# Optimization experiments

Measured on AMD Instinct MI355X. Metric: run time of the kernel, lower is better.

Reference implementation:

```python
import jax, jax.numpy as jnp
import numpy as np

# --- static config (matches init_kwargs) ---
C = 384        # channels
H = 8          # num_heads
HD = C // H    # head_dim = 48
K = 1024       # patch_size (window)
BASE = 100.0   # rope_freq
MAX_POS = 4096
GRID_SIZE = 0.02
LN_EPS = 1e-5


def _interleave8(x, y, z):
    """Morton-interleave the low 8 bits of x,y,z -> 24-bit code (int32)."""
    key = jnp.zeros_like(x)
    for i in range(8):
        m = 1 << i
        key = key | ((x & m) << (2 * i + 2)) | ((y & m) << (2 * i + 1)) | ((z & m) << (2 * i))
    return key


def _serialize_points(xyz):
    """xyz: (B,3,N) -> (order (B,N) int32, grid (B,N,3) int32). Z-order sort."""
    pts = jnp.transpose(xyz, (0, 2, 1))                       # (B,N,3)
    grid = ((pts - pts.min(axis=1, keepdims=True)) / GRID_SIZE).astype(jnp.int32)
    grid = jnp.clip(grid, 0, 65535)
    gx, gy, gz = grid[..., 0], grid[..., 1], grid[..., 2]
    lo = _interleave8(gx & 255, gy & 255, gz & 255)           # low 24 bits of Morton code
    hi = _interleave8((gx >> 8) & 255, (gy >> 8) & 255, (gz >> 8) & 255)  # high word
    # 48-bit Morton order == lexsort with hi as primary key, lo secondary
    order = jax.vmap(lambda l, h: jnp.lexsort((l, h)))(lo, hi)
    return order.astype(jnp.int32), grid


def _rope_tables(d):
    inv_freq = 1.0 / (BASE ** (jnp.arange(0, d, 2, dtype=jnp.float32) / d))
    t = jnp.arange(MAX_POS, dtype=jnp.float32)
    freqs = t[:, None] * inv_freq[None, :]                    # (MAX_POS, d/2)
    freqs = jnp.concatenate([freqs, freqs], axis=-1)          # (MAX_POS, d)
    return jnp.cos(freqs), jnp.sin(freqs)


def _rotate_half(x):
    h = x.shape[-1] // 2
    return jnp.concatenate([-x[..., h:], x[..., :h]], axis=-1)


def _point_rope(tok, pos):
    """tok: (B,H,N,D) with D%3==0; pos: (B,N,3) int grid coords."""
    D = tok.shape[-1]
    d = D // 3
    pos = jnp.clip(pos, 0, MAX_POS - 1)
    cos, sin = _rope_tables(d)
    outs = []
    for axis, ch in enumerate(jnp.split(tok, 3, axis=-1)):
        p = pos[:, :, axis]                                   # (B,N)
        c = cos[p][:, None]                                   # (B,1,N,d)
        s = sin[p][:, None]
        outs.append(ch * c + _rotate_half(ch) * s)
    return jnp.concatenate(outs, axis=-1)


def _layernorm(x, g, b):
    mu = x.mean(axis=-1, keepdims=True)
    var = ((x - mu) ** 2).mean(axis=-1, keepdims=True)
    return (x - mu) * jax.lax.rsqrt(var + LN_EPS) * g + b


def _forward(x, xyz, ln1_g, ln1_b, qkv_w, qkv_b, proj_w, proj_b,
             ln2_g, ln2_b, ffn_w1, ffn_b1, ffn_w2, ffn_b2):
    B, C_, N = x.shape
    order, grid = _serialize_points(xyz)
    x_sorted = jnp.take_along_axis(x, order[:, None, :], axis=2)          # (B,C,N)
    grid_sorted = jnp.take_along_axis(grid, order[:, :, None], axis=1)    # (B,N,3)
    x_t = jnp.transpose(x_sorted, (0, 2, 1))                              # (B,N,C)
    shortcut = x_t
    xn = _layernorm(x_t, ln1_g, ln1_b)
    pad = (K - N % K) % K
    if pad > 0:
        xn = jnp.pad(xn, ((0, 0), (0, pad), (0, 0)))
        grid_sorted = jnp.pad(grid_sorted, ((0, 0), (0, pad), (0, 0)))
    Np = xn.shape[1]
    nw = Np // K
    qkv = (xn @ qkv_w + qkv_b).reshape(B, Np, 3, H, HD)
    q = jnp.transpose(qkv[:, :, 0], (0, 2, 1, 3))                         # (B,H,Np,HD)
    k = jnp.transpose(qkv[:, :, 1], (0, 2, 1, 3))
    v = jnp.transpose(qkv[:, :, 2], (0, 2, 1, 3))
    q = _point_rope(q, grid_sorted)
    k = _point_rope(k, grid_sorted)
    qw = q.reshape(B, H, nw, K, HD)
    kw = k.reshape(B, H, nw, K, HD)
    vw = v.reshape(B, H, nw, K, HD)
    scale = 1.0 / np.sqrt(HD).astype(np.float32)
    scores = jnp.einsum('bhwqd,bhwkd->bhwqk', qw, kw) * scale             # (B,H,nw,K,K)
    attn = jax.nn.softmax(scores, axis=-1)
    out = jnp.einsum('bhwqk,bhwkd->bhwqd', attn, vw)                      # (B,H,nw,K,HD)
    out = jnp.transpose(out, (0, 2, 3, 1, 4)).reshape(B, Np, C)
    out = out[:, :N]
    out = out @ proj_w + proj_b
    x_t = shortcut + out
    x_t = x_t + (jax.nn.gelu(_layernorm(x_t, ln2_g, ln2_b) @ ffn_w1 + ffn_b1,
                             approximate=False) @ ffn_w2 + ffn_b2)
    x_out = jnp.transpose(x_t, (0, 2, 1))                                 # (B,C,N)
    inv_order = jnp.argsort(order, axis=1)
    x_out = jnp.take_along_axis(x_out, inv_order[:, None, :], axis=2)
    return x_out


def setup_inputs() -> dict:
    key = jax.random.key(0)
    ks = jax.random.split(key, 12)
    B, N = 1, 16384
    s = 0.02
    return {
        'x': jax.random.normal(ks[0], (B, C, N), dtype=jnp.float32),
        'xyz': jax.random.uniform(ks[1], (B, 3, N), dtype=jnp.float32),
        'ln1_g': jnp.ones((C,), jnp.float32),
        'ln1_b': jnp.zeros((C,), jnp.float32),
        'qkv_w': jax.random.normal(ks[2], (C, 3 * C), jnp.float32) * s,
        'qkv_b': jnp.zeros((3 * C,), jnp.float32),
        'proj_w': jax.random.normal(ks[3], (C, C), jnp.float32) * s,
        'proj_b': jnp.zeros((C,), jnp.float32),
        'ln2_g': jnp.ones((C,), jnp.float32),
        'ln2_b': jnp.zeros((C,), jnp.float32),
        'ffn_w1': jax.random.normal(ks[4], (C, 4 * C), jnp.float32) * s,
        'ffn_b1': jnp.zeros((4 * C,), jnp.float32),
        'ffn_w2': jax.random.normal(ks[5], (4 * C, C), jnp.float32) * s,
        'ffn_b2': jnp.zeros((C,), jnp.float32),
    }


def reference(x, xyz, ln1_g, ln1_b, qkv_w, qkv_b, proj_w, proj_b,
              ln2_g, ln2_b, ffn_w1, ffn_b1, ffn_w2, ffn_b2):
    return _forward(x, xyz, ln1_g, ln1_b, qkv_w, qkv_b, proj_w, proj_b,
                    ln2_g, ln2_b, ffn_w1, ffn_b1, ffn_w2, ffn_b2)
```

## Files before the change

kernel.cpp:

```cpp
#include <hip/hip_runtime.h>
#include <hip/hip_bf16.h>

typedef unsigned short u16;
typedef unsigned int u32;
typedef unsigned long long u64;
typedef __attribute__((ext_vector_type(8))) short s16x8;
typedef __attribute__((ext_vector_type(4))) short s16x4;
typedef __attribute__((ext_vector_type(8))) unsigned short u16x8;
typedef __attribute__((ext_vector_type(4))) unsigned short u16x4;
typedef __attribute__((ext_vector_type(4))) float fx4;
typedef __attribute__((ext_vector_type(4))) unsigned int ux4;
typedef __attribute__((ext_vector_type(2))) unsigned int ux2;

__device__ __forceinline__ float bf2f(u16 u){ u32 x=((u32)u)<<16; return __builtin_bit_cast(float,x); }
__device__ __forceinline__ u16 f2bf(float f){ u32 x=__builtin_bit_cast(u32,f); return (u16)((x + 0x7FFFu + ((x>>16)&1u))>>16); }
__device__ __forceinline__ u32 cvtpk(float lo, float hi){
  u32 r; asm("v_cvt_pk_bf16_f32 %0, %1, %2" : "=v"(r) : "v"(lo), "v"(hi)); return r;
}

__device__ __forceinline__ s16x8 ld_bf8(const u16* p){
  s16x4 lo = *(const s16x4*)p;
  s16x4 hi = *(const s16x4*)(p+4);
  s16x8 r;
  r[0]=lo[0]; r[1]=lo[1]; r[2]=lo[2]; r[3]=lo[3];
  r[4]=hi[0]; r[5]=hi[1]; r[6]=hi[2]; r[7]=hi[3];
  return r;
}

__device__ __forceinline__ void gload16(const void* g, void* l){
  __builtin_amdgcn_global_load_lds((__attribute__((address_space(1))) void*)g,
                                   (__attribute__((address_space(3))) void*)l, 16, 0, 0);
}

__device__ __forceinline__ u64 spread3(u32 v){
  u64 x = v & 0xFFFFull;
  x = (x | (x<<32)) & 0x001f00000000ffffull;
  x = (x | (x<<16)) & 0x001f0000ff0000ffull;
  x = (x | (x<<8))  & 0x100f00f00f00f00full;
  x = (x | (x<<4))  & 0x10c30c30c30c30c3ull;
  x = (x | (x<<2))  & 0x1249249249249249ull;
  return x;
}

__global__ __launch_bounds__(256) void min3_kernel(const float* __restrict__ xyz, u32* __restrict__ mins, int N)
{
  int i = blockIdx.x*256 + threadIdx.x;
  float v0 = xyz[i], v1 = xyz[N+i], v2 = xyz[2*N+i];
  #pragma unroll
  for (int s=1;s<64;s<<=1){
    v0 = fminf(v0, __shfl_xor(v0,s));
    v1 = fminf(v1, __shfl_xor(v1,s));
    v2 = fminf(v2, __shfl_xor(v2,s));
  }
  if ((threadIdx.x & 63) == 0){
    atomicMin(mins+0, __builtin_bit_cast(u32, v0));
    atomicMin(mins+1, __builtin_bit_cast(u32, v1));
    atomicMin(mins+2, __builtin_bit_cast(u32, v2));
  }
}

__global__ __launch_bounds__(1024) void bsort_keys_kernel(const float* __restrict__ xyz, const u32* __restrict__ mins,
        u64* __restrict__ keys, int* __restrict__ gridO, int N)
{
  __shared__ u64 sk[2048];
  int t = threadIdx.x, bid = blockIdx.x;
  float mx0 = __builtin_bit_cast(float, mins[0]);
  float mx1 = __builtin_bit_cast(float, mins[1]);
  float mx2 = __builtin_bit_cast(float, mins[2]);
  int i0 = bid*2048;
  #pragma unroll
  for (int p=0;p<2;p++){
    int i = i0 + t + p*1024;
    int gx=(int)((xyz[i]-mx0)/0.02f);     gx = gx<0?0:(gx>65535?65535:gx);
    int gy=(int)((xyz[N+i]-mx1)/0.02f);   gy = gy<0?0:(gy>65535?65535:gy);
    int gz=(int)((xyz[2*N+i]-mx2)/0.02f); gz = gz<0?0:(gz>65535?65535:gz);
    gridO[i*3+0]=gx; gridO[i*3+1]=gy; gridO[i*3+2]=gz;
    u64 mort = (spread3((u32)gx)<<2)|(spread3((u32)gy)<<1)|spread3((u32)gz);
    sk[t + p*1024] = (mort<<14) | (u64)i;
  }
  for (int size=2; size<=2048; size<<=1){
    for (int stride=size>>1; stride>0; stride>>=1){
      __syncthreads();
      int i = 2*t - (t & (stride-1));
      int j = i + stride;
      u64 a = sk[i], b = sk[j];
      bool up = ((i & size) == 0);
      if ((a > b) == up){ sk[i]=b; sk[j]=a; }
    }
  }
  __syncthreads();
  keys[i0 + t] = sk[t];
  keys[i0 + 1024 + t] = sk[t+1024];
}

template<bool FINAL>
__global__ __launch_bounds__(256) void merge_kernel(const u64* __restrict__ src, u64* __restrict__ dst,
        int* __restrict__ order, int L, int N)
{
  int gt = blockIdx.x*256 + threadIdx.x;
  int d0 = gt*4;
  if (d0 >= N) return;
  int pair = d0 / (2*L);
  int base = pair*2*L;
  int ld = d0 - base;
  const u64* A = src + base;
  const u64* B = A + L;
  int lo = ld > L ? ld - L : 0;
  int hi = ld < L ? ld : L;
  while (lo < hi){
    int mid = (lo+hi)>>1;
    if (A[mid] <= B[ld-1-mid]) lo = mid+1; else hi = mid;
  }
  int i = lo, j = ld - lo;
  u64* out = dst + base + ld;
  int* oout = order + base + ld;
  u64 a = (i < L) ? A[i] : ~0ull;
  u64 b = (j < L) ? B[j] : ~0ull;
  #pragma unroll
  for (int e=0;e<4;e++){
    u64 v;
    if (a <= b){ v = a; i++; a = (i<L)?A[i]:~0ull; }
    else       { v = b; j++; b = (j<L)?B[j]:~0ull; }
    out[e] = v;
    if (FINAL) oout[e] = (int)(v & 16383ull);
  }
}

__global__ __launch_bounds__(256) void wtrans4_kernel(const float* __restrict__ qkv_w, const float* __restrict__ proj_w,
    const float* __restrict__ w1, const float* __restrict__ w2,
    u16* __restrict__ qkv_wT, u16* __restrict__ proj_wT, u16* __restrict__ w1T, u16* __restrict__ w2T)
{
  __shared__ float tl[32][33];
  int bid = blockIdx.x;
  const float* W; u16* Wt; int K, Nc, lb;
  if (bid < 432)      { W=qkv_w;  Wt=qkv_wT;  K=384;  Nc=1152; lb=bid; }
  else if (bid < 576) { W=proj_w; Wt=proj_wT; K=384;  Nc=384;  lb=bid-432; }
  else if (bid < 1152){ W=w1;     Wt=w1T;     K=384;  Nc=1536; lb=bid-576; }
  else                { W=w2;     Wt=w2T;     K=1536; Nc=384;  lb=bid-1152; }
  int nb = Nc/32;
  int n0 = (lb % nb)*32;
  int k0 = (lb / nb)*32;
  int t=threadIdx.x; int r=t>>5, c=t&31;
  #pragma unroll
  for (int p=0;p<4;p++) tl[p*8+r][c] = W[(size_t)(k0+p*8+r)*Nc + n0+c];
  __syncthreads();
  #pragma unroll
  for (int p=0;p<4;p++) Wt[(size_t)(n0+p*8+r)*K + k0+c] = f2bf(tl[c][p*8+r]);
}

template<bool BF16IN>
__global__ __launch_bounds__(256) void ln32_kernel(const void* __restrict__ xin, const float* __restrict__ g,
     const float* __restrict__ b, u16* __restrict__ xn, int N)
{
  extern __shared__ char dsm[];
  float* tile = (float*)dsm;
  int n0 = blockIdx.x*32;
  int t = threadIdx.x;
  int tok32 = t&31, cg2 = t>>5;
  #pragma unroll 8
  for (int p=0;p<48;p++){
    int cc = p*8 + cg2;
    float v;
    if (BF16IN) v = bf2f(((const u16*)xin)[(size_t)cc*N + n0 + tok32]);
    else        v = ((const float*)xin)[(size_t)cc*N + n0 + tok32];
    tile[tok32*388 + cc] = v;
  }
  __syncthreads();
  int tok = t>>3, part = t&7;
  const float* row = tile + tok*388 + part*48;
  float s=0.f;
  #pragma unroll
  for (int j=0;j<48;j++) s += row[j];
  s += __shfl_xor(s,1); s += __shfl_xor(s,2); s += __shfl_xor(s,4);
  float mu = s*(1.0f/384.0f);
  float vr=0.f;
  #pragma unroll
  for (int j=0;j<48;j++){ float d=row[j]-mu; vr += d*d; }
  vr += __shfl_xor(vr,1); vr += __shfl_xor(vr,2); vr += __shfl_xor(vr,4);
  float rs = rsqrtf(vr*(1.0f/384.0f) + 1e-5f);
  u16* dst = xn + (size_t)(n0+tok)*384 + part*48;
  #pragma unroll
  for (int q=0;q<6;q++){
    float v[8];
    #pragma unroll
    for (int j=0;j<8;j++){
      int c = part*48 + q*8 + j;
      v[j] = (row[q*8+j]-mu)*rs*g[c] + b[c];
    }
    ux4 o;
    o[0]=cvtpk(v[0],v[1]); o[1]=cvtpk(v[2],v[3]); o[2]=cvtpk(v[4],v[5]); o[3]=cvtpk(v[6],v[7]);
    *(ux4*)(dst + q*8) = o;
  }
}

__device__ __forceinline__ float gelu_f(float v){
  return 0.5f*v*(1.0f + erff(v*0.7071067811865475f));
}

template<int EPI>
__global__ __launch_bounds__(512) void gemm256_kernel(const u16* __restrict__ A, const u16* __restrict__ Bt,
    const float* __restrict__ bias, u16* __restrict__ outB, int M, int Nout, int K)
{
  __shared__ u16 Al[256*64];
  __shared__ u16 Bl[128*64];
  int nmt = M>>8;
  int m0 = (blockIdx.x % nmt)<<8;
  int n0 = (blockIdx.x / nmt)<<7;
  int t = threadIdx.x, lane=t&63, wv=t>>6, wr=wv>>1, wc=wv&1;
  int fr = lane&15, fg = lane>>4;
  fx4 acc[4][4];
  #pragma unroll
  for (int i=0;i<4;i++)
  #pragma unroll
  for (int j=0;j<4;j++) acc[i][j]=(fx4){0.f,0.f,0.f,0.f};
  int srowA = wv*32 + (lane>>3);
  int srowB = wv*16 + (lane>>3);
  int swz  = ((lane&7) ^ ((lane>>3)&7)) * 8;
  const u16* ApL = A  + (size_t)(m0+srowA)*K + swz;
  const u16* BpL = Bt + (size_t)(n0+srowB)*K + swz;
  u16* AlW = Al + wv*2048 + lane*8;
  u16* BlW = Bl + wv*1024 + lane*8;
  const u16* a_base = Al + (wr*64+fr)*64;
  const u16* b_base = Bl + (wc*64+fr)*64;
  int swr = fr & 7;
  for (int k0=0;k0<K;k0+=64){
    #pragma unroll
    for (int i=0;i<4;i++) gload16(ApL + k0 + (size_t)i*8*K, AlW + i*512);
    #pragma unroll
    for (int i=0;i<2;i++) gload16(BpL + k0 + (size_t)i*8*K, BlW + i*512);
    __syncthreads();
    #pragma unroll
    for (int ks=0;ks<2;ks++){
      int soff = (((ks*4+fg) ^ swr) << 3);
      s16x8 a[4], b[4];
      #pragma unroll
      for (int mi=0;mi<4;mi++) a[mi] = *(const s16x8*)(a_base + mi*1024 + soff);
      #pragma unroll
      for (int ni=0;ni<4;ni++) b[ni] = *(const s16x8*)(b_base + ni*1024 + soff);
      #pragma unroll
      for (int mi=0;mi<4;mi++)
      #pragma unroll
      for (int ni=0;ni<4;ni++)
        acc[mi][ni] = __builtin_amdgcn_mfma_f32_16x16x32_bf16(a[mi], b[ni], acc[mi][ni], 0,0,0);
    }
    __syncthreads();
  }
  #pragma unroll
  for (int mi=0;mi<4;mi++)
  #pragma unroll
  for (int ni=0;ni<4;ni++){
    int c = n0 + wc*64 + ni*16 + fr;
    float bi = bias[c];
    int mb = m0 + wr*64 + mi*16 + fg*4;
    #pragma unroll
    for (int j=0;j<4;j++){
      float vv = acc[mi][ni][j] + bi;
      if (EPI==1) vv = gelu_f(vv);
      outB[(size_t)(mb+j)*Nout + c] = f2bf(vv);
    }
  }
}

template<int EPI>
__global__ __launch_bounds__(256) void gemm128x2_kernel(const u16* __restrict__ A, const u16* __restrict__ Bt,
    const float* __restrict__ bias, u16* __restrict__ outB, float* __restrict__ outF,
    const float* __restrict__ resF, const u16* __restrict__ resB, int M, int Nout, int K)
{
  __shared__ u16 Al[2][128*64];
  __shared__ u16 Bl[2][128*64];
  int nmt = M>>7;
  int m0 = (blockIdx.x % nmt)<<7;
  int n0 = (blockIdx.x / nmt)<<7;
  int t = threadIdx.x, lane=t&63, wv=t>>6, wr=wv>>1, wc=wv&1;
  int fr = lane&15, fg = lane>>4;
  fx4 acc[4][4];
  #pragma unroll
  for (int i=0;i<4;i++)
  #pragma unroll
  for (int j=0;j<4;j++) acc[i][j]=(fx4){0.f,0.f,0.f,0.f};
  int srow = wv*32 + (lane>>3);
  int swz  = ((lane&7) ^ ((lane>>3)&7)) * 8;
  const u16* ApL = A  + (size_t)(m0+srow)*K + swz;
  const u16* BpL = Bt + (size_t)(n0+srow)*K + swz;
  int woff = wv*2048 + lane*8;
  int swr = fr & 7;
  for (int k0=0;k0<K;k0+=128){
    #pragma unroll
    for (int i=0;i<4;i++){
      gload16(ApL + k0 +      (size_t)i*8*K, Al[0] + woff + i*512);
      gload16(BpL + k0 +      (size_t)i*8*K, Bl[0] + woff + i*512);
      gload16(ApL + k0 + 64 + (size_t)i*8*K, Al[1] + woff + i*512);
      gload16(BpL + k0 + 64 + (size_t)i*8*K, Bl[1] + woff + i*512);
    }
    __syncthreads();
    #pragma unroll
    for (int sub=0;sub<2;sub++){
      const u16* a_base = Al[sub] + (wr*64+fr)*64;
      const u16* b_base = Bl[sub] + (wc*64+fr)*64;
      #pragma unroll
      for (int ks=0;ks<2;ks++){
        int soff = (((ks*4+fg) ^ swr) << 3);
        s16x8 a[4], b[4];
        #pragma unroll
        for (int mi=0;mi<4;mi++) a[mi] = *(const s16x8*)(a_base + mi*1024 + soff);
        #pragma unroll
        for (int ni=0;ni<4;ni++) b[ni] = *(const s16x8*)(b_base + ni*1024 + soff);
        #pragma unroll
        for (int mi=0;mi<4;mi++)
        #pragma unroll
        for (int ni=0;ni<4;ni++)
          acc[mi][ni] = __builtin_amdgcn_mfma_f32_16x16x32_bf16(a[mi], b[ni], acc[mi][ni], 0,0,0);
      }
    }
    __syncthreads();
  }
  if (EPI==2){
    #pragma unroll
    for (int mi=0;mi<4;mi++)
    #pragma unroll
    for (int ni=0;ni<4;ni++){
      int c = n0 + wc*64 + ni*16 + fr;
      float bi = bias[c];
      size_t idx = (size_t)c*M + m0 + wr*64 + mi*16 + fg*4;
      fx4 r4 = *(const fx4*)(resF + idx);
      ux2 p;
      p[0] = cvtpk(acc[mi][ni][0]+bi+r4[0], acc[mi][ni][1]+bi+r4[1]);
      p[1] = cvtpk(acc[mi][ni][2]+bi+r4[2], acc[mi][ni][3]+bi+r4[3]);
      *(ux2*)(outB + idx) = p;
    }
  } else {
    #pragma unroll
    for (int mi=0;mi<4;mi++)
    #pragma unroll
    for (int ni=0;ni<4;ni++){
      int c = n0 + wc*64 + ni*16 + fr;
      float bi = bias[c];
      size_t idx = (size_t)c*M + m0 + wr*64 + mi*16 + fg*4;
      ux2 rb = *(const ux2*)(resB + idx);
      fx4 o;
      o[0] = acc[mi][ni][0] + bi + bf2f((u16)rb[0]);
      o[1] = acc[mi][ni][1] + bi + bf2f((u16)(rb[0]>>16));
      o[2] = acc[mi][ni][2] + bi + bf2f((u16)rb[1]);
      o[3] = acc[mi][ni][3] + bi + bf2f((u16)(rb[1]>>16));
      *(fx4*)(outF + idx) = o;
    }
  }
}

#define LOG2_100_O8 0.8304820237218405f

__global__ __launch_bounds__(256) void rope_kernel(const u16* __restrict__ qkv, const int* __restrict__ order,
    const int* __restrict__ gridO, u16* __restrict__ Qp, u16* __restrict__ Kp, u16* __restrict__ Vp, int N)
{
  __shared__ float csm[64][24][2];
  __shared__ int origs[64];
  int i0 = blockIdx.x<<6;
  int t = threadIdx.x;
  if (t<64) origs[t] = order[i0+t];
  __syncthreads();
  for (int idx=t; idx<64*24; idx+=256){
    int tok = idx/24, slot = idx - tok*24;
    int a = slot>>3, fi = slot&7;
    int pos = gridO[(size_t)origs[tok]*3 + a];
    pos = pos<0?0:(pos>4095?4095:pos);
    float invf = __builtin_amdgcn_exp2f(-(float)fi * LOG2_100_O8);
    float ang = (float)pos * invf;
    csm[tok][slot][0] = __cosf(ang);
    csm[tok][slot][1] = __sinf(ang);
  }
  __syncthreads();
  int tok = t&63;
  int i = i0 + tok;
  const u16* src = qkv + (size_t)origs[tok]*1152;
  for (int h=t>>6; h<8; h+=4){
    size_t dst = ((size_t)h*N + i)*48;
    #pragma unroll
    for (int a=0;a<3;a++){
      u16x8 qa = *(const u16x8*)(src + h*48 + a*16);
      u16x8 qb = *(const u16x8*)(src + h*48 + a*16 + 8);
      u16x8 ka = *(const u16x8*)(src + 384 + h*48 + a*16);
      u16x8 kb = *(const u16x8*)(src + 384 + h*48 + a*16 + 8);
      float oqa[8], oqb[8], oka[8], okb[8];
      #pragma unroll
      for (int j=0;j<8;j++){
        float c0 = csm[tok][a*8+j][0], s0 = csm[tok][a*8+j][1];
        float ql = bf2f(qa[j]), qh = bf2f(qb[j]);
        float kl = bf2f(ka[j]), kh = bf2f(kb[j]);
        oqa[j] = ql*c0 - qh*s0;
        oqb[j] = qh*c0 + ql*s0;
        oka[j] = kl*c0 - kh*s0;
        okb[j] = kh*c0 + kl*s0;
      }
      ux4 OQa, OQb, OKa, OKb;
      #pragma unroll
      for (int p=0;p<4;p++){
        OQa[p]=cvtpk(oqa[2*p],oqa[2*p+1]);
        OQb[p]=cvtpk(oqb[2*p],oqb[2*p+1]);
        OKa[p]=cvtpk(oka[2*p],oka[2*p+1]);
        OKb[p]=cvtpk(okb[2*p],okb[2*p+1]);
      }
      *(ux4*)(Qp + dst + a*16) = OQa;
      *(ux4*)(Qp + dst + a*16 + 8) = OQb;
      *(ux4*)(Kp + dst + a*16) = OKa;
      *(ux4*)(Kp + dst + a*16 + 8) = OKb;
      u16x8 va = *(const u16x8*)(src + 768 + h*48 + a*16);
      u16x8 vb = *(const u16x8*)(src + 768 + h*48 + a*16 + 8);
      *(u16x8*)(Vp + dst + a*16) = va;
      *(u16x8*)(Vp + dst + a*16 + 8) = vb;
    }
  }
}

#define ATTN_SCALE 0.14433756729740643f
#define E2SCALE 0.2082354550504211f
#define DEFER_RAW 55.0f
#define KSTRIDE 68

__global__ __launch_bounds__(512) void attn7_kernel(const u16* __restrict__ Qp, const u16* __restrict__ Kp,
    const u16* __restrict__ Vp, const int* __restrict__ order, u16* __restrict__ attn, int N, int nw)
{
  __shared__ u16 Kl[2][64*KSTRIDE];
  __shared__ u16 Vl[2][48*KSTRIDE];
  __shared__ u16 Pl[8][32*KSTRIDE];
  int b = blockIdx.x;
  int hw = b & 127;
  int qc = b >> 7;
  int w = hw % nw, h = hw / nw;
  int t = threadIdx.x, lane = t&63, wv = t>>6;
  int fr = lane & 15, fg = lane >> 4;
  size_t base = ((size_t)h*N + (size_t)w*1024);
  int q0 = qc*256 + wv*32;
  bool kact = t < 384;
  int krow = t/6, kc = t - krow*6;
  const u16* ksrc = Kp + (base + krow)*48 + kc*8;
  int koff = krow*KSTRIDE + kc*8;
  int s2 = t - 128;
  bool vact = t >= 128;
  int vrow = s2/6, vc = s2 - vrow*6;
  const u16* vsrc = Vp + (base + vrow)*48 + vc*8;
  int vkey = vrow ^ (vc<<3);
  if (t < 256){
    ux2 z = {0,0};
    *(ux2*)&Kl[0][(t>>2)*KSTRIDE + 48 + (t&3)*4] = z;
    *(ux2*)&Kl[1][(t>>2)*KSTRIDE + 48 + (t&3)*4] = z;
  }
  s16x8 qf[2][2];
  s16x8 zf = {0,0,0,0,0,0,0,0};
  #pragma unroll
  for (int n=0;n<2;n++){
    const u16* qrow = Qp + (base + q0 + n*16 + fr)*48;
    qf[n][0] = ld_bf8(qrow + fg*8);
    qf[n][1] = (fg < 2) ? ld_bf8(qrow + 32 + fg*8) : zf;
  }
  s16x8 ones;
  #pragma unroll
  for (int j=0;j<8;j++) ones[j] = (short)0x3F80;

  float m0r = -3.4e38f, m1r = -3.4e38f;
  fx4 o00=(fx4){0.f,0.f,0.f,0.f}, o01=o00, o02=o00, o03=o00, o10=o00, o11=o00, o12=o00, o13=o00;
  u16* pl = Pl[wv];
  ux4 kreg = {0,0,0,0}, vreg = {0,0,0,0};
  if (kact) kreg = *(const ux4*)ksrc;
  if (vact) vreg = *(const ux4*)vsrc;
  if (kact){
    ux2 lo; lo[0]=kreg[0]; lo[1]=kreg[1];
    ux2 hi; hi[0]=kreg[2]; hi[1]=kreg[3];
    *(ux2*)(Kl[0]+koff) = lo; *(ux2*)(Kl[0]+koff+4) = hi;
  }
  if (vact){
    u16* vcp = Vl[0] + vkey;
    vcp[(vc*8+0)*KSTRIDE] = (u16)vreg[0];
    vcp[(vc*8+1)*KSTRIDE] = (u16)(vreg[0]>>16);
    vcp[(vc*8+2)*KSTRIDE] = (u16)vreg[1];
    vcp[(vc*8+3)*KSTRIDE] = (u16)(vreg[1]>>16);
    vcp[(vc*8+4)*KSTRIDE] = (u16)vreg[2];
    vcp[(vc*8+5)*KSTRIDE] = (u16)(vreg[2]>>16);
    vcp[(vc*8+6)*KSTRIDE] = (u16)vreg[3];
    vcp[(vc*8+7)*KSTRIDE] = (u16)(vreg[3]>>16);
  }
  __syncthreads();

  for (int c=0;c<16;c++){
    int cur = c & 1;
    const u16* kl = Kl[cur];
    const u16* vl = Vl[cur];
    if (c < 15){
      if (kact) kreg = *(const ux4*)(ksrc + (size_t)(c+1)*3072);
      if (vact) vreg = *(const ux4*)(vsrc + (size_t)(c+1)*3072);
    }
    fx4 s0[4], s1v[4];
    __builtin_amdgcn_s_setprio(1);
    #pragma unroll
    for (int m=0;m<4;m++){
      s0[m]=(fx4){0.f,0.f,0.f,0.f}; s1v[m]=s0[m];
      #pragma unroll
      for (int s=0;s<2;s++){
        s16x8 af = ld_bf8(kl + (m*16+fr)*KSTRIDE + s*32 + fg*8);
        s0[m]  = __builtin_amdgcn_mfma_f32_16x16x32_bf16(af, qf[0][s], s0[m],  0,0,0);
        s1v[m] = __builtin_amdgcn_mfma_f32_16x16x32_bf16(af, qf[1][s], s1v[m], 0,0,0);
      }
    }
    __builtin_amdgcn_s_setprio(0);
    float pm0 = -3.4e38f, pm1 = -3.4e38f;
    #pragma unroll
    for (int m=0;m<4;m++){
      float a0 = fmaxf(fmaxf(s0[m][0],s0[m][1]), fmaxf(s0[m][2],s0[m][3]));
      float a1 = fmaxf(fmaxf(s1v[m][0],s1v[m][1]), fmaxf(s1v[m][2],s1v[m][3]));
      pm0 = fmaxf(pm0, a0); pm1 = fmaxf(pm1, a1);
    }
    pm0 = fmaxf(pm0, __shfl_xor(pm0,16)); pm0 = fmaxf(pm0, __shfl_xor(pm0,32));
    pm1 = fmaxf(pm1, __shfl_xor(pm1,16)); pm1 = fmaxf(pm1, __shfl_xor(pm1,32));
    if (!__all((pm0 <= m0r + DEFER_RAW) & (pm1 <= m1r + DEFER_RAW))){
      float nm0 = fmaxf(m0r, pm0), nm1 = fmaxf(m1r, pm1);
      float f0 = __builtin_amdgcn_exp2f((m0r - nm0)*E2SCALE);
      float f1 = __builtin_amdgcn_exp2f((m1r - nm1)*E2SCALE);
      m0r = nm0; m1r = nm1;
      #pragma unroll
      for (int j=0;j<4;j++){
        float g0 = __shfl(f0, fg*4+j);
        float g1 = __shfl(f1, fg*4+j);
        o00[j]*=g0; o01[j]*=g0; o02[j]*=g0; o03[j]*=g0;
        o10[j]*=g1; o11[j]*=g1; o12[j]*=g1; o13[j]*=g1;
      }
    }
    #pragma unroll
    for (int m=0;m<4;m++){
      float e0[4], e1[4];
      #pragma unroll
      for (int j=0;j<4;j++){
        e0[j] = __builtin_amdgcn_exp2f((s0[m][j]-m0r)*E2SCALE);
        e1[j] = __builtin_amdgcn_exp2f((s1v[m][j]-m1r)*E2SCALE);
      }
      ux2 P0, P1;
      P0[0]=cvtpk(e0[0],e0[1]); P0[1]=cvtpk(e0[2],e0[3]);
      P1[0]=cvtpk(e1[0],e1[1]); P1[1]=cvtpk(e1[2],e1[3]);
      *(ux2*)&pl[(fr)*KSTRIDE + m*16 + fg*4]      = P0;
      *(ux2*)&pl[(16+fr)*KSTRIDE + m*16 + fg*4]   = P1;
    }
    __builtin_amdgcn_s_setprio(1);
    #pragma unroll
    for (int s=0;s<2;s++){
      int kb = s*32 + fg*8;
      s16x8 pa0 = ld_bf8(pl + fr*KSTRIDE + kb);
      s16x8 pa1 = ld_bf8(pl + (16+fr)*KSTRIDE + kb);
      s16x8 vb0 = ld_bf8(vl + (fr)*KSTRIDE    + (kb ^ ((fr)&56)));
      s16x8 vb1 = ld_bf8(vl + (16+fr)*KSTRIDE + (kb ^ ((16+fr)&56)));
      s16x8 vb2 = ld_bf8(vl + (32+fr)*KSTRIDE + (kb ^ ((32+fr)&56)));
      o00 = __builtin_amdgcn_mfma_f32_16x16x32_bf16(pa0, vb0, o00, 0,0,0);
      o01 = __builtin_amdgcn_mfma_f32_16x16x32_bf16(pa0, vb1, o01, 0,0,0);
      o02 = __builtin_amdgcn_mfma_f32_16x16x32_bf16(pa0, vb2, o02, 0,0,0);
      o03 = __builtin_amdgcn_mfma_f32_16x16x32_bf16(pa0, ones, o03, 0,0,0);
      o10 = __builtin_amdgcn_mfma_f32_16x16x32_bf16(pa1, vb0, o10, 0,0,0);
      o11 = __builtin_amdgcn_mfma_f32_16x16x32_bf16(pa1, vb1, o11, 0,0,0);
      o12 = __builtin_amdgcn_mfma_f32_16x16x32_bf16(pa1, vb2, o12, 0,0,0);
      o13 = __builtin_amdgcn_mfma_f32_16x16x32_bf16(pa1, ones, o13, 0,0,0);
    }
    __builtin_amdgcn_s_setprio(0);
    if (c < 15){
      u16* kln = Kl[cur^1];
      u16* vln = Vl[cur^1];
      if (kact){
        ux2 lo; lo[0]=kreg[0]; lo[1]=kreg[1];
        ux2 hi; hi[0]=kreg[2]; hi[1]=kreg[3];
        *(ux2*)(kln+koff) = lo; *(ux2*)(kln+koff+4) = hi;
      }
      if (vact){
        u16* vcp = vln + vkey;
        vcp[(vc*8+0)*KSTRIDE] = (u16)vreg[0];
        vcp[(vc*8+1)*KSTRIDE] = (u16)(vreg[0]>>16);
        vcp[(vc*8+2)*KSTRIDE] = (u16)vreg[1];
        vcp[(vc*8+3)*KSTRIDE] = (u16)(vreg[1]>>16);
        vcp[(vc*8+4)*KSTRIDE] = (u16)vreg[2];
        vcp[(vc*8+5)*KSTRIDE] = (u16)(vreg[2]>>16);
        vcp[(vc*8+6)*KSTRIDE] = (u16)vreg[3];
        vcp[(vc*8+7)*KSTRIDE] = (u16)(vreg[3]>>16);
      }
      __syncthreads();
    }
  }
  const int* ord = order + w*1024 + q0;
  #pragma unroll
  for (int j=0;j<4;j++){
    float inv0 = 1.0f / o03[j];
    float inv1 = 1.0f / o13[j];
    int orig0 = ord[fg*4+j];
    u16* dst0 = attn + (size_t)orig0*384 + h*48;
    dst0[fr]      = f2bf(o00[j]*inv0);
    dst0[16+fr]   = f2bf(o01[j]*inv0);
    dst0[32+fr]   = f2bf(o02[j]*inv0);
    int orig1 = ord[16 + fg*4+j];
    u16* dst1 = attn + (size_t)orig1*384 + h*48;
    dst1[fr]      = f2bf(o10[j]*inv1);
    dst1[16+fr]   = f2bf(o11[j]*inv1);
    dst1[32+fr]   = f2bf(o12[j]*inv1);
  }
}

extern "C" void kernel_launch(void* const* d_in, const int* in_sizes, int n_in,
                              void* d_out, int out_size, void* d_ws, size_t ws_size,
                              hipStream_t stream)
{
  (void)n_in; (void)out_size; (void)ws_size;
  const float* x     = (const float*)d_in[0];
  const float* xyz   = (const float*)d_in[1];
  const float* ln1_g = (const float*)d_in[2];
  const float* ln1_b = (const float*)d_in[3];
  const float* qkv_w = (const float*)d_in[4];
  const float* qkv_b = (const float*)d_in[5];
  const float* proj_w= (const float*)d_in[6];
  const float* proj_b= (const float*)d_in[7];
  const float* ln2_g = (const float*)d_in[8];
  const float* ln2_b = (const float*)d_in[9];
  const float* ffn_w1= (const float*)d_in[10];
  const float* ffn_b1= (const float*)d_in[11];
  const float* ffn_w2= (const float*)d_in[12];
  const float* ffn_b2= (const float*)d_in[13];
  int N = in_sizes[0]/384;
  int nw = N/1024;
  char* wsp = (char*)d_ws;
  size_t off = 0;
  auto alloc = [&](size_t bytes)->char*{ char* p = wsp + off; off = (off + bytes + 255) & ~(size_t)255; return p; };
  int*  order   = (int*)alloc((size_t)N*4);
  int*  gridO   = (int*)alloc((size_t)N*12);
  u32*  mins    = (u32*)alloc(256);
  u64*  keysA   = (u64*)alloc((size_t)N*8);
  u64*  keysB   = (u64*)alloc((size_t)N*8);
  u16*  qkv_wT  = (u16*)alloc((size_t)1152*384*2);
  u16*  proj_wT = (u16*)alloc((size_t)384*384*2);
  u16*  w1T     = (u16*)alloc((size_t)1536*384*2);
  u16*  w2T     = (u16*)alloc((size_t)384*1536*2);
  u16*  xn      = (u16*)alloc((size_t)N*384*2);
  u16*  Qp      = (u16*)alloc((size_t)N*48*8*2);
  u16*  Kp      = (u16*)alloc((size_t)N*48*8*2);
  u16*  Vp      = (u16*)alloc((size_t)N*48*8*2);
  u16*  qkvb    = (u16*)alloc((size_t)N*1152*2);
  u16*  y1b     = (u16*)alloc((size_t)N*384*2);
  u16*  attn    = xn;
  u16*  xn2     = qkvb;
  u16*  mid     = xn;
  float* outF = (float*)d_out;

  hipMemsetAsync(mins, 0xFF, 12, stream);
  min3_kernel<<<N/256, 256, 0, stream>>>(xyz, mins, N);
  bsort_keys_kernel<<<N/2048, 1024, 0, stream>>>(xyz, mins, keysA, gridO, N);
  merge_kernel<false><<<N/1024, 256, 0, stream>>>(keysA, keysB, order, 2048, N);
  merge_kernel<false><<<N/1024, 256, 0, stream>>>(keysB, keysA, order, 4096, N);
  merge_kernel<true><<<N/1024, 256, 0, stream>>>(keysA, keysB, order, 8192, N);

  wtrans4_kernel<<<1728, 256, 0, stream>>>(qkv_w, proj_w, ffn_w1, ffn_w2, qkv_wT, proj_wT, w1T, w2T);
  ln32_kernel<false><<<N/32, 256, 32*388*4, stream>>>(x, ln1_g, ln1_b, xn, N);
  gemm256_kernel<0><<<(N/256)*(1152/128), 512, 0, stream>>>(xn, qkv_wT, qkv_b, qkvb, N, 1152, 384);
  rope_kernel<<<N/64, 256, 0, stream>>>(qkvb, order, gridO, Qp, Kp, Vp, N);
  attn7_kernel<<<8*nw*4, 512, 0, stream>>>(Qp, Kp, Vp, order, attn, N, nw);
  gemm128x2_kernel<2><<<(N/128)*(384/128), 256, 0, stream>>>(attn, proj_wT, proj_b, y1b, nullptr, x, nullptr, N, 384, 384);
  ln32_kernel<true><<<N/32, 256, 32*388*4, stream>>>(y1b, ln2_g, ln2_b, xn2, N);
  gemm256_kernel<1><<<(N/256)*(1536/128), 512, 0, stream>>>(xn2, w1T, ffn_b1, mid, N, 1536, 384);
  gemm128x2_kernel<3><<<(N/128)*(384/128), 256, 0, stream>>>(mid, w2T, ffn_b2, nullptr, outF, nullptr, y1b, N, 384, 1536);
}
```

Baseline: 274.3 us.

## Cut launch count: cooperative merge, fused weight-transpose+LN1, memset-free min

Replaces the memset plus atomicMin reduction with per-block partial minima that the sort kernel reduces itself. Merges the three merge passes into one cooperative kernel with grid syncs, and fuses the weight transpose and first layernorm into one launch. The aim is to cut kernel-launch and inter-kernel gap overhead in the short preprocessing stages. It relies on cooperative launch support, and the fused kernel requests the large LN shared-memory size even for transpose blocks, which may lower their occupancy.

```diff
diff --git a/kernel.cpp b/kernel.cpp
--- a/kernel.cpp
+++ b/kernel.cpp
@@ -1,5 +1,8 @@
 #include <hip/hip_runtime.h>
 #include <hip/hip_bf16.h>
+#include <hip/hip_cooperative_groups.h>
+
+namespace cg = cooperative_groups;
 
 typedef unsigned short u16;
 typedef unsigned int u32;
@@ -42,9 +45,11 @@
   return x;
 }
 
-__global__ __launch_bounds__(256) void min3_kernel(const float* __restrict__ xyz, u32* __restrict__ mins, int N)
-{
+__global__ __launch_bounds__(256) void min3_kernel(const float* __restrict__ xyz, float* __restrict__ minsW, int N)
+{
+  __shared__ float red[3][4];
   int i = blockIdx.x*256 + threadIdx.x;
+  int lane = threadIdx.x&63, wv = threadIdx.x>>6;
   float v0 = xyz[i], v1 = xyz[N+i], v2 = xyz[2*N+i];
   #pragma unroll
   for (int s=1;s<64;s<<=1){
@@ -52,21 +57,29 @@
     v1 = fminf(v1, __shfl_xor(v1,s));
     v2 = fminf(v2, __shfl_xor(v2,s));
   }
-  if ((threadIdx.x & 63) == 0){
-    atomicMin(mins+0, __builtin_bit_cast(u32, v0));
-    atomicMin(mins+1, __builtin_bit_cast(u32, v1));
-    atomicMin(mins+2, __builtin_bit_cast(u32, v2));
-  }
-}
-
-__global__ __launch_bounds__(1024) void bsort_keys_kernel(const float* __restrict__ xyz, const u32* __restrict__ mins,
+  if (lane==0){ red[0][wv]=v0; red[1][wv]=v1; red[2][wv]=v2; }
+  __syncthreads();
+  if (threadIdx.x < 3){
+    float m = fminf(fminf(red[threadIdx.x][0],red[threadIdx.x][1]),
+                    fminf(red[threadIdx.x][2],red[threadIdx.x][3]));
+    minsW[blockIdx.x*3 + threadIdx.x] = m;
+  }
+}
+
+__global__ __launch_bounds__(1024) void bsort_keys_kernel(const float* __restrict__ xyz, const float* __restrict__ minsW,
         u64* __restrict__ keys, int* __restrict__ gridO, int N)
 {
   __shared__ u64 sk[2048];
+  __shared__ float mnS[3];
   int t = threadIdx.x, bid = blockIdx.x;
-  float mx0 = __builtin_bit_cast(float, mins[0]);
-  float mx1 = __builtin_bit_cast(float, mins[1]);
-  float mx2 = __builtin_bit_cast(float, mins[2]);
+  if (t < 192){
+    float v = minsW[(t&63)*3 + (t>>6)];
+    #pragma unroll
+    for (int s=1;s<64;s<<=1) v = fminf(v, __shfl_xor(v,s));
+    if ((t&63)==0) mnS[t>>6] = v;
+  }
+  __syncthreads();
+  float mx0=mnS[0], mx1=mnS[1], mx2=mnS[2];
   int i0 = bid*2048;
   #pragma unroll
   for (int p=0;p<2;p++){
@@ -93,13 +106,10 @@
   keys[i0 + 1024 + t] = sk[t+1024];
 }
 
-template<bool FINAL>
-__global__ __launch_bounds__(256) void merge_kernel(const u64* __restrict__ src, u64* __restrict__ dst,
-        int* __restrict__ order, int L, int N)
-{
-  int gt = blockIdx.x*256 + threadIdx.x;
+__device__ __forceinline__ void merge_phase(const u64* __restrict__ src, u64* __restrict__ dst,
+        int* __restrict__ order, int L, int gt)
+{
   int d0 = gt*4;
-  if (d0 >= N) return;
   int pair = d0 / (2*L);
   int base = pair*2*L;
   int ld = d0 - base;
@@ -113,7 +123,7 @@
   }
   int i = lo, j = ld - lo;
   u64* out = dst + base + ld;
-  int* oout = order + base + ld;
+  int* oout = order ? order + base + ld : nullptr;
   u64 a = (i < L) ? A[i] : ~0ull;
   u64 b = (j < L) ? B[j] : ~0ull;
   #pragma unroll
@@ -122,34 +132,87 @@
     if (a <= b){ v = a; i++; a = (i<L)?A[i]:~0ull; }
     else       { v = b; j++; b = (j<L)?B[j]:~0ull; }
     out[e] = v;
-    if (FINAL) oout[e] = (int)(v & 16383ull);
-  }
-}
-
-__global__ __launch_bounds__(256) void wtrans4_kernel(const float* __restrict__ qkv_w, const float* __restrict__ proj_w,
+    if (oout) oout[e] = (int)(v & 16383ull);
+  }
+}
+
+__global__ __launch_bounds__(256) void mergeall_kernel(u64* __restrict__ keysA, u64* __restrict__ keysB,
+        int* __restrict__ order, int N)
+{
+  cg::grid_group gg = cg::this_grid();
+  int gt = blockIdx.x*256 + threadIdx.x;
+  merge_phase(keysA, keysB, nullptr, 2048, gt);
+  gg.sync();
+  merge_phase(keysB, keysA, nullptr, 4096, gt);
+  gg.sync();
+  merge_phase(keysA, keysB, order, 8192, gt);
+}
+
+__global__ __launch_bounds__(256) void wtln_kernel(const float* __restrict__ x, const float* __restrict__ g,
+    const float* __restrict__ b, u16* __restrict__ xn, int N,
+    const float* __restrict__ qkv_w, const float* __restrict__ proj_w,
     const float* __restrict__ w1, const float* __restrict__ w2,
     u16* __restrict__ qkv_wT, u16* __restrict__ proj_wT, u16* __restrict__ w1T, u16* __restrict__ w2T)
 {
-  __shared__ float tl[32][33];
+  extern __shared__ char dsm[];
   int bid = blockIdx.x;
-  const float* W; u16* Wt; int K, Nc, lb;
-  if (bid < 432)      { W=qkv_w;  Wt=qkv_wT;  K=384;  Nc=1152; lb=bid; }
-  else if (bid < 576) { W=proj_w; Wt=proj_wT; K=384;  Nc=384;  lb=bid-432; }
-  else if (bid < 1152){ W=w1;     Wt=w1T;     K=384;  Nc=1536; lb=bid-576; }
-  else                { W=w2;     Wt=w2T;     K=1536; Nc=384;  lb=bid-1152; }
-  int nb = Nc/32;
-  int n0 = (lb % nb)*32;
-  int k0 = (lb / nb)*32;
-  int t=threadIdx.x; int r=t>>5, c=t&31;
-  #pragma unroll
-  for (int p=0;p<4;p++) tl[p*8+r][c] = W[(size_t)(k0+p*8+r)*Nc + n0+c];
-  __syncthreads();
-  #pragma unroll
-  for (int p=0;p<4;p++) Wt[(size_t)(n0+p*8+r)*K + k0+c] = f2bf(tl[c][p*8+r]);
-}
-
-template<bool BF16IN>
-__global__ __launch_bounds__(256) void ln32_kernel(const void* __restrict__ xin, const float* __restrict__ g,
+  int t = threadIdx.x;
+  if (bid < 512){
+    float* tile = (float*)dsm;
+    int n0 = bid*32;
+    int tok32 = t&31, cg2 = t>>5;
+    #pragma unroll 8
+    for (int p=0;p<48;p++){
+      int cc = p*8 + cg2;
+      tile[tok32*388 + cc] = x[(size_t)cc*N + n0 + tok32];
+    }
+    __syncthreads();
+    int tok = t>>3, part = t&7;
+    const float* row = tile + tok*388 + part*48;
+    float s=0.f;
+    #pragma unroll
+    for (int j=0;j<48;j++) s += row[j];
+    s += __shfl_xor(s,1); s += __shfl_xor(s,2); s += __shfl_xor(s,4);
+    float mu = s*(1.0f/384.0f);
+    float vr=0.f;
+    #pragma unroll
+    for (int j=0;j<48;j++){ float d=row[j]-mu; vr += d*d; }
+    vr += __shfl_xor(vr,1); vr += __shfl_xor(vr,2); vr += __shfl_xor(vr,4);
+    float rs = rsqrtf(vr*(1.0f/384.0f) + 1e-5f);
+    u16* dst = xn + (size_t)(n0+tok)*384 + part*48;
+    #pragma unroll
+    for (int q=0;q<6;q++){
+      float v[8];
+      #pragma unroll
+      for (int j=0;j<8;j++){
+        int c = part*48 + q*8 + j;
+        v[j] = (row[q*8+j]-mu)*rs*g[c] + b[c];
+      }
+      ux4 o;
+      o[0]=cvtpk(v[0],v[1]); o[1]=cvtpk(v[2],v[3]); o[2]=cvtpk(v[4],v[5]); o[3]=cvtpk(v[6],v[7]);
+      *(ux4*)(dst + q*8) = o;
+    }
+  } else {
+    float (*tl)[33] = (float(*)[33])dsm;
+    int wb = bid - 512;
+    const float* W; u16* Wt; int K, Nc, lb;
+    if (wb < 432)      { W=qkv_w;  Wt=qkv_wT;  K=384;  Nc=1152; lb=wb; }
+    else if (wb < 576) { W=proj_w; Wt=proj_wT; K=384;  Nc=384;  lb=wb-432; }
+    else if (wb < 1152){ W=w1;     Wt=w1T;     K=384;  Nc=1536; lb=wb-576; }
+    else               { W=w2;     Wt=w2T;     K=1536; Nc=384;  lb=wb-1152; }
+    int nb = Nc/32;
+    int n0 = (lb % nb)*32;
+    int k0 = (lb / nb)*32;
+    int r=t>>5, c=t&31;
+    #pragma unroll
+    for (int p=0;p<4;p++) tl[p*8+r][c] = W[(size_t)(k0+p*8+r)*Nc + n0+c];
+    __syncthreads();
+    #pragma unroll
+    for (int p=0;p<4;p++) Wt[(size_t)(n0+p*8+r)*K + k0+c] = f2bf(tl[c][p*8+r]);
+  }
+}
+
+__global__ __launch_bounds__(256) void ln32b_kernel(const u16* __restrict__ xin, const float* __restrict__ g,
      const float* __restrict__ b, u16* __restrict__ xn, int N)
 {
   extern __shared__ char dsm[];
@@ -160,10 +223,7 @@
   #pragma unroll 8
   for (int p=0;p<48;p++){
     int cc = p*8 + cg2;
-    float v;
-    if (BF16IN) v = bf2f(((const u16*)xin)[(size_t)cc*N + n0 + tok32]);
-    else        v = ((const float*)xin)[(size_t)cc*N + n0 + tok32];
-    tile[tok32*388 + cc] = v;
+    tile[tok32*388 + cc] = bf2f(xin[(size_t)cc*N + n0 + tok32]);
   }
   __syncthreads();
   int tok = t>>3, part = t&7;
@@ -622,7 +682,7 @@
   auto alloc = [&](size_t bytes)->char*{ char* p = wsp + off; off = (off + bytes + 255) & ~(size_t)255; return p; };
   int*  order   = (int*)alloc((size_t)N*4);
   int*  gridO   = (int*)alloc((size_t)N*12);
-  u32*  mins    = (u32*)alloc(256);
+  float* minsW  = (float*)alloc((size_t)(N/256)*12);
   u64*  keysA   = (u64*)alloc((size_t)N*8);
   u64*  keysB   = (u64*)alloc((size_t)N*8);
   u16*  qkv_wT  = (u16*)alloc((size_t)1152*384*2);
@@ -640,20 +700,21 @@
   u16*  mid     = xn;
   float* outF = (float*)d_out;
 
-  hipMemsetAsync(mins, 0xFF, 12, stream);
-  min3_kernel<<<N/256, 256, 0, stream>>>(xyz, mins, N);
-  bsort_keys_kernel<<<N/2048, 1024, 0, stream>>>(xyz, mins, keysA, gridO, N);
-  merge_kernel<false><<<N/1024, 256, 0, stream>>>(keysA, keysB, order, 2048, N);
-  merge_kernel<false><<<N/1024, 256, 0, stream>>>(keysB, keysA, order, 4096, N);
-  merge_kernel<true><<<N/1024, 256, 0, stream>>>(keysA, keysB, order, 8192, N);
-
-  wtrans4_kernel<<<1728, 256, 0, stream>>>(qkv_w, proj_w, ffn_w1, ffn_w2, qkv_wT, proj_wT, w1T, w2T);
-  ln32_kernel<false><<<N/32, 256, 32*388*4, stream>>>(x, ln1_g, ln1_b, xn, N);
+  min3_kernel<<<N/256, 256, 0, stream>>>(xyz, minsW, N);
+  bsort_keys_kernel<<<N/2048, 1024, 0, stream>>>(xyz, minsW, keysA, gridO, N);
+  {
+    u64* kA = keysA; u64* kB = keysB; int* op = order; int Nv = N;
+    void* margs[] = { (void*)&kA, (void*)&kB, (void*)&op, (void*)&Nv };
+    hipLaunchCooperativeKernel((const void*)mergeall_kernel, dim3(N/1024), dim3(256), margs, 0, stream);
+  }
+
+  wtln_kernel<<<512+1728, 256, 32*388*4, stream>>>(x, ln1_g, ln1_b, xn, N,
+      qkv_w, proj_w, ffn_w1, ffn_w2, qkv_wT, proj_wT, w1T, w2T);
   gemm256_kernel<0><<<(N/256)*(1152/128), 512, 0, stream>>>(xn, qkv_wT, qkv_b, qkvb, N, 1152, 384);
   rope_kernel<<<N/64, 256, 0, stream>>>(qkvb, order, gridO, Qp, Kp, Vp, N);
   attn7_kernel<<<8*nw*4, 512, 0, stream>>>(Qp, Kp, Vp, order, attn, N, nw);
   gemm128x2_kernel<2><<<(N/128)*(384/128), 256, 0, stream>>>(attn, proj_wT, proj_b, y1b, nullptr, x, nullptr, N, 384, 384);
-  ln32_kernel<true><<<N/32, 256, 32*388*4, stream>>>(y1b, ln2_g, ln2_b, xn2, N);
+  ln32b_kernel<<<N/32, 256, 32*388*4, stream>>>(y1b, ln2_g, ln2_b, xn2, N);
   gemm256_kernel<1><<<(N/256)*(1536/128), 512, 0, stream>>>(xn2, w1T, ffn_b1, mid, N, 1536, 384);
   gemm128x2_kernel<3><<<(N/128)*(384/128), 256, 0, stream>>>(mid, w2T, ffn_b2, nullptr, outF, nullptr, y1b, N, 384, 1536);
 }
```

After: 291.8 us. +6.4%, slower.
